# Optimization experiments

Hardware: AMD Instinct MI355X
Metric: run time of the kernel (lower is better)

The kernel has to match this reference:

```python
import jax, jax.numpy as jnp
import numpy as np

B, N, FEAT = 64, 1024, 3
HID, STATE, LAYERS, NTYPES = 64, 32, 2, 10


def setup_inputs() -> dict:
    key = jax.random.key(0)
    ks = jax.random.split(key, 16)
    s = 0.1
    return {
        "task_features": jax.random.normal(ks[0], (B, N, FEAT), jnp.float32),
        "task_types": jax.random.randint(ks[1], (B, N), 0, NTYPES, jnp.int32),
        "prev_state": jnp.zeros((B, STATE), jnp.float32),
        "enc_w1": jax.random.normal(ks[2], (HID, FEAT), jnp.float32) * s,
        "enc_b1": jnp.zeros((HID,), jnp.float32),
        "enc_w2": jax.random.normal(ks[3], (HID, HID), jnp.float32) * s,
        "enc_b2": jnp.zeros((HID,), jnp.float32),
        "contention": jax.random.normal(ks[4], (NTYPES, NTYPES), jnp.float32) * 0.1,
        "gnn_w": jax.random.normal(ks[5], (LAYERS, HID, HID), jnp.float32) * s,
        "gnn_b": jnp.zeros((LAYERS, HID), jnp.float32),
        "gru_w_ih": jax.random.normal(ks[6], (3 * STATE, HID), jnp.float32) * s,
        "gru_w_hh": jax.random.normal(ks[7], (3 * STATE, STATE), jnp.float32) * s,
        "gru_b_ih": jnp.zeros((3 * STATE,), jnp.float32),
        "gru_b_hh": jnp.zeros((3 * STATE,), jnp.float32),
        "head_w1": jax.random.normal(ks[8], (HID, HID + STATE), jnp.float32) * s,
        "head_b1": jnp.zeros((HID,), jnp.float32),
        "head_w2": jax.random.normal(ks[9], (1, HID), jnp.float32) * s,
        "head_b2": jnp.zeros((1,), jnp.float32),
    }


def _forward(task_features, task_types, prev_state, enc_w1, enc_b1, enc_w2, enc_b2,
             contention, gnn_w, gnn_b, gru_w_ih, gru_w_hh, gru_b_ih, gru_b_hh,
             head_w1, head_b1, head_w2, head_b2):
    # task encoder: Linear -> ReLU -> Linear
    emb = jax.nn.relu(task_features @ enc_w1.T + enc_b1) @ enc_w2.T + enc_b2  # (B,N,H)
    # interaction graph: type-pair gather + cosine similarity
    base = contention[task_types[:, :, None], task_types[:, None, :]]  # (B,N,N)
    nrm = emb / jnp.maximum(jnp.linalg.norm(emb, axis=-1, keepdims=True), 1e-12)
    sim = jnp.einsum("bnd,bmd->bnm", nrm, nrm)
    adjacency = jax.nn.sigmoid(base) * sim  # (B,N,N)
    # GNN layers: aggregate + linear + relu
    h = emb
    for l in range(LAYERS):
        agg = jnp.einsum("bnm,bmd->bnd", adjacency, h)
        h = jax.nn.relu((h + agg) @ gnn_w[l].T + gnn_b[l])
    ctx = h.mean(axis=1)  # (B,H)
    # GRUCell (torch semantics)
    gi = ctx @ gru_w_ih.T + gru_b_ih
    gh = prev_state @ gru_w_hh.T + gru_b_hh
    i_r, i_z, i_n = jnp.split(gi, 3, axis=-1)
    h_r, h_z, h_n = jnp.split(gh, 3, axis=-1)
    r = jax.nn.sigmoid(i_r + h_r)
    z = jax.nn.sigmoid(i_z + h_z)
    n = jnp.tanh(i_n + r * h_n)
    new_state = (1.0 - z) * n + z * prev_state  # (B,S)
    # latency head on [h, state]
    st = jnp.broadcast_to(new_state[:, None, :], (h.shape[0], h.shape[1], new_state.shape[-1]))
    combined = jnp.concatenate([h, st], axis=-1)
    lat = jax.nn.relu(combined @ head_w1.T + head_b1) @ head_w2.T + head_b2
    return lat[..., 0], new_state


def reference(task_features, task_types, prev_state, enc_w1, enc_b1, enc_w2, enc_b2,
              contention, gnn_w, gnn_b, gru_w_ih, gru_w_hh, gru_b_ih, gru_b_hh,
              head_w1, head_b1, head_w2, head_b2):
    return _forward(task_features, task_types, prev_state, enc_w1, enc_b1, enc_w2, enc_b2,
                    contention, gnn_w, gnn_b, gru_w_ih, gru_w_hh, gru_b_ih, gru_b_hh,
                    head_w1, head_b1, head_w2, head_b2)
```

## Files before the change

kernel.cpp:

```cpp
#include <hip/hip_runtime.h>
#include <math.h>

#define BB 64
#define NN 1024
#define HID 64
#define STATE 32
#define NTYPES 10
#define CAP 256
#define CAPE (CAP * 64)

typedef _Float16 f16;
typedef f16 f16x8 __attribute__((ext_vector_type(8)));
typedef f16 f16x4 __attribute__((ext_vector_type(4)));
typedef float f32x4 __attribute__((ext_vector_type(4)));

#define MFMA16(a, b, c) __builtin_amdgcn_mfma_f32_16x16x32_f16(a, b, c, 0, 0, 0)

__device__ __forceinline__ float sigm(float x) { return 1.f / (1.f + expf(-x)); }

__device__ __forceinline__ f16x8 cvt8(float4 a, float4 b) {
    f16x8 r;
    r[0] = (f16)a.x; r[1] = (f16)a.y; r[2] = (f16)a.z; r[3] = (f16)a.w;
    r[4] = (f16)b.x; r[5] = (f16)b.y; r[6] = (f16)b.z; r[7] = (f16)b.w;
    return r;
}
__device__ __forceinline__ unsigned packh2(f16 a, f16 b) {
    union { f16 h[2]; unsigned u; } p;
    p.h[0] = a; p.h[1] = b;
    return p.u;
}

__device__ __forceinline__ void swz_load(const float* __restrict__ W, int K, int n,
                                         f16* dst, int tid) {
    for (int p = tid; p < n; p += 256) {
        int j = p & 7, ln = (p >> 3) & 63, nt = (p >> 9) & 3, ch = p >> 11;
        int k = ch * 32 + ((ln >> 4) << 3) + j;
        int o = nt * 16 + (ln & 15);
        dst[p] = (f16)W[o * K + k];
    }
}

__global__ __launch_bounds__(256) void k_encoder(
    const float* __restrict__ feat,
    const float* __restrict__ w1, const float* __restrict__ b1,
    const float* __restrict__ w2, const float* __restrict__ b2,
    const int* __restrict__ types, int* __restrict__ idx, int* __restrict__ cnt,
    f16* __restrict__ nrmp, float* __restrict__ sclp, float* __restrict__ ctx)
{
    __shared__ f16 w2s[4096];
    __shared__ f16 tmp[4][16 * 72];
    __shared__ float fbuf[4][48];
    __shared__ int pkbuf[64];
    int tid = threadIdx.x, wave = tid >> 6, lane = tid & 63;
    int l15 = lane & 15, quad = lane >> 4;
    if (tid < 64) {
        int row = blockIdx.x * 64 + tid;
        int b = row >> 10;
        int t = types[row];
        int bt = b * NTYPES + t;
        int pos = atomicAdd(&cnt[bt], 1);
        idx[bt * CAP + pos] = row & (NN - 1);
        pkbuf[tid] = bt * CAP + pos;
    }
    if (blockIdx.x < 16) ctx[blockIdx.x * 256 + tid] = 0.f;
    swz_load(w2, 64, 4096, w2s, tid);
    float w10 = w1[lane * 3], w11 = w1[lane * 3 + 1], w12 = w1[lane * 3 + 2], b1l = b1[lane];
    int tb = blockIdx.x * 64 + wave * 16;
    if (lane < 48) fbuf[wave][lane] = feat[tb * 3 + lane];
    __syncthreads();
    f16* tw = &tmp[wave][0];
#pragma unroll
    for (int r = 0; r < 16; ++r) {
        float x0 = fbuf[wave][r * 3], x1 = fbuf[wave][r * 3 + 1], x2 = fbuf[wave][r * 3 + 2];
        float hv = fmaxf(fmaf(w10, x0, fmaf(w11, x1, fmaf(w12, x2, b1l))), 0.f);
        tw[r * 72 + lane] = (f16)hv;
    }
    __builtin_amdgcn_sched_barrier(0);
    f16x8 a0 = *(const f16x8*)&tw[l15 * 72 + quad * 8];
    f16x8 a1 = *(const f16x8*)&tw[l15 * 72 + 32 + quad * 8];
    const f16x8* bf = (const f16x8*)w2s;
    f32x4 acc[4];
#pragma unroll
    for (int nt = 0; nt < 4; ++nt) {
        f32x4 c = {0.f, 0.f, 0.f, 0.f};
        c = MFMA16(a0, bf[(0 * 4 + nt) * 64 + lane], c);
        c = MFMA16(a1, bf[(1 * 4 + nt) * 64 + lane], c);
        acc[nt] = c;
    }
    float b2c[4];
#pragma unroll
    for (int nt = 0; nt < 4; ++nt) b2c[nt] = b2[nt * 16 + l15];
#pragma unroll
    for (int i = 0; i < 4; ++i) {
        float v[4]; float ss = 0.f;
#pragma unroll
        for (int nt = 0; nt < 4; ++nt) { v[nt] = acc[nt][i] + b2c[nt]; ss = fmaf(v[nt], v[nt], ss); }
        ss += __shfl_xor(ss, 1, 64); ss += __shfl_xor(ss, 2, 64);
        ss += __shfl_xor(ss, 4, 64); ss += __shfl_xor(ss, 8, 64);
        float nm = fmaxf(sqrtf(ss), 1e-12f);
        float rinv = 1.f / nm;
        int pk = pkbuf[wave * 16 + quad * 4 + i];
#pragma unroll
        for (int nt = 0; nt < 4; ++nt)
            nrmp[(size_t)pk * 64 + nt * 16 + l15] = (f16)(v[nt] * rinv);
        if (l15 == 0) sclp[pk] = nm;
    }
}

#define TSTR2 72
__global__ __launch_bounds__(256) void k_buildM0(
    const int* __restrict__ cnt, const f16* __restrict__ nrmp,
    const float* __restrict__ sclp, f16* __restrict__ M0)
{
    __shared__ f16 nT[64 * TSTR2];
    __shared__ f16 hT[64 * TSTR2];
    int i0 = blockIdx.x;
    int xcd = i0 & 7, kk = i0 >> 3;
    int b = xcd + 8 * (kk / NTYPES);
    int t = kk % NTYPES;
    int bt = b * NTYPES + t;
    int c = cnt[bt];
    int tid = threadIdx.x, wave = tid >> 6, lane = tid & 63;
    int l15 = lane & 15, quad = lane >> 4;
    int r = tid & 15, q4 = tid >> 4;
    const f16* nb = nrmp + (size_t)bt * CAPE;
    const float* sb = sclp + (size_t)bt * CAP;
    f32x4 acc[4] = {{0.f,0.f,0.f,0.f},{0.f,0.f,0.f,0.f},{0.f,0.f,0.f,0.f},{0.f,0.f,0.f,0.f}};
    for (int k0 = 0; k0 < c; k0 += 64) {
        __syncthreads();
        f16x4 a[4], g[4];
#pragma unroll
        for (int u = 0; u < 4; ++u) { a[u] = (f16x4){0,0,0,0}; g[u] = (f16x4){0,0,0,0}; }
#pragma unroll
        for (int u = 0; u < 4; ++u) {
            int mi = k0 + 4 * r + u;
            if (mi < c) {
                a[u] = *(const f16x4*)&nb[(size_t)mi * 64 + 4 * q4];
                f16 sm = (f16)sb[mi]; f16x4 sv = {sm, sm, sm, sm};
                g[u] = a[u] * sv;
            }
        }
#pragma unroll
        for (int i = 0; i < 4; ++i) {
            *(unsigned*)&nT[(4 * q4 + i) * TSTR2 + 4 * r]     = packh2(a[0][i], a[1][i]);
            *(unsigned*)&nT[(4 * q4 + i) * TSTR2 + 4 * r + 2] = packh2(a[2][i], a[3][i]);
            *(unsigned*)&hT[(4 * q4 + i) * TSTR2 + 4 * r]     = packh2(g[0][i], g[1][i]);
            *(unsigned*)&hT[(4 * q4 + i) * TSTR2 + 4 * r + 2] = packh2(g[2][i], g[3][i]);
        }
        __syncthreads();
        f16x8 af0 = *(const f16x8*)&nT[(wave * 16 + l15) * TSTR2 + quad * 8];
        f16x8 af1 = *(const f16x8*)&nT[(wave * 16 + l15) * TSTR2 + 32 + quad * 8];
#pragma unroll
        for (int nt = 0; nt < 4; ++nt) {
            f16x8 bf0 = *(const f16x8*)&hT[(nt * 16 + l15) * TSTR2 + quad * 8];
            f16x8 bf1 = *(const f16x8*)&hT[(nt * 16 + l15) * TSTR2 + 32 + quad * 8];
            acc[nt] = MFMA16(af0, bf0, acc[nt]);
            acc[nt] = MFMA16(af1, bf1, acc[nt]);
        }
    }
    f16* Mo = M0 + (size_t)bt * 4096;
#pragma unroll
    for (int nt = 0; nt < 4; ++nt)
#pragma unroll
        for (int i = 0; i < 4; ++i)
            Mo[(wave * 16 + quad * 4 + i) * 64 + nt * 16 + l15] = (f16)acc[nt][i];
}

__global__ __launch_bounds__(256) void k_gnn0_fused(
    const int* __restrict__ cnt, const float* __restrict__ cont,
    const f16* __restrict__ M, const f16* __restrict__ nrmp,
    const float* __restrict__ sclp,
    const float* __restrict__ gw, const float* __restrict__ gb,
    f16* __restrict__ h1p, f16* __restrict__ Mout)
{
    __shared__ f16 ds_[4096];
    __shared__ f16 gs[4096];
    __shared__ __align__(16) f16 nT[64 * TSTR2];
    __shared__ __align__(16) f16 hT[64 * TSTR2];
    int i0 = blockIdx.x;
    int xcd = i0 & 7, kk = i0 >> 3;
    int b = xcd + 8 * (kk / NTYPES);
    int t = kk % NTYPES;
    int bt = b * NTYPES + t;
    int c = cnt[bt];
    int tid = threadIdx.x, wave = tid >> 6, lane = tid & 63;
    int l15 = lane & 15, quad = lane >> 4;
    swz_load(gw, 64, 4096, gs, tid);
    float sg[NTYPES];
#pragma unroll
    for (int j = 0; j < NTYPES; ++j) sg[j] = sigm(cont[t * NTYPES + j]);
    float ca[16];
#pragma unroll
    for (int i = 0; i < 16; ++i) ca[i] = 0.f;
    const f16* Mb = M + (size_t)b * NTYPES * 4096;
#pragma unroll
    for (int j = 0; j < NTYPES; ++j) {
        const f16* Mr = Mb + j * 4096 + (wave * 16 + l15) * 64;
        f16x8 m0 = *(const f16x8*)&Mr[quad * 8];
        f16x8 m1 = *(const f16x8*)&Mr[32 + quad * 8];
        float sv = sg[j];
#pragma unroll
        for (int e = 0; e < 8; ++e) {
            ca[e]     = fmaf(sv, (float)m0[e], ca[e]);
            ca[8 + e] = fmaf(sv, (float)m1[e], ca[8 + e]);
        }
    }
    f16x8 ca0, ca1;
#pragma unroll
    for (int i = 0; i < 8; ++i) { ca0[i] = (f16)ca[i]; ca1[i] = (f16)ca[8 + i]; }
    __syncthreads();
    const f16x8* gbf = (const f16x8*)gs;
#pragma unroll
    for (int nt = 0; nt < 4; ++nt) {
        f32x4 dd = {0.f, 0.f, 0.f, 0.f};
        dd = MFMA16(ca0, gbf[(0 * 4 + nt) * 64 + lane], dd);
        dd = MFMA16(ca1, gbf[(1 * 4 + nt) * 64 + lane], dd);
#pragma unroll
        for (int i = 0; i < 4; ++i) {
            int d = wave * 16 + quad * 4 + i;
            int pos = (((d >> 5) * 4 + nt) * 64 + ((d >> 3) & 3) * 16 + l15) * 8 + (d & 7);
            ds_[pos] = (f16)dd[i];
        }
    }
    __syncthreads();
    float gbl[4];
#pragma unroll
    for (int nt = 0; nt < 4; ++nt) gbl[nt] = gb[nt * 16 + l15];
    const f16* nb = nrmp + (size_t)bt * CAPE;
    const float* sb = sclp + (size_t)bt * CAP;
    f16* hob = h1p + (size_t)bt * CAPE;
    const f16x8* dbf = (const f16x8*)ds_;
    f32x4 macc[4];
#pragma unroll
    for (int nt = 0; nt < 4; ++nt) macc[nt] = (f32x4){0.f, 0.f, 0.f, 0.f};
    int nchunk = (c + 63) >> 6;
    for (int ch = 0; ch < nchunk; ++ch) {
        int tb = ch * 64 + wave * 16;
        int rA = tb + l15;
        bool okA = rA < c;
        int rAc = okA ? rA : (c - 1);
        const f16* na = nb + (size_t)rAc * 64;
        f16x8 a0 = *(const f16x8*)&na[quad * 8];
        f16x8 a1 = *(const f16x8*)&na[32 + quad * 8];
        f32x4 acc1[4], acc2[4];
#pragma unroll
        for (int nt = 0; nt < 4; ++nt) {
            f32x4 c1 = {0.f, 0.f, 0.f, 0.f}, c2 = {0.f, 0.f, 0.f, 0.f};
            c1 = MFMA16(a0, dbf[(0 * 4 + nt) * 64 + lane], c1);
            c1 = MFMA16(a1, dbf[(1 * 4 + nt) * 64 + lane], c1);
            c2 = MFMA16(a0, gbf[(0 * 4 + nt) * 64 + lane], c2);
            c2 = MFMA16(a1, gbf[(1 * 4 + nt) * 64 + lane], c2);
            acc1[nt] = c1; acc2[nt] = c2;
        }
        f16x4 hv[4];
#pragma unroll
        for (int nt = 0; nt < 4; ++nt) hv[nt] = (f16x4){0, 0, 0, 0};
#pragma unroll
        for (int i = 0; i < 4; ++i) {
            int rr = tb + quad * 4 + i;
            if (rr < c) {
                float sm = sb[rr];
#pragma unroll
                for (int nt = 0; nt < 4; ++nt) {
                    float v = fmaxf(fmaf(sm, acc2[nt][i], acc1[nt][i]) + gbl[nt], 0.f);
                    f16 vh = (f16)v;
                    hob[(size_t)rr * 64 + nt * 16 + l15] = vh;
                    hv[nt][i] = vh;
                }
            }
        }
        f16x8 z8 = {0, 0, 0, 0, 0, 0, 0, 0};
        f16x8 s0 = okA ? a0 : z8;
        f16x8 s1 = okA ? a1 : z8;
#pragma unroll
        for (int j = 0; j < 8; ++j) {
            nT[(quad * 8 + j) * TSTR2 + wave * 16 + l15]      = s0[j];
            nT[(32 + quad * 8 + j) * TSTR2 + wave * 16 + l15] = s1[j];
        }
#pragma unroll
        for (int nt = 0; nt < 4; ++nt)
            *(f16x4*)&hT[(nt * 16 + l15) * TSTR2 + wave * 16 + quad * 4] = hv[nt];
        __syncthreads();
        f16x8 af0 = *(const f16x8*)&nT[(wave * 16 + l15) * TSTR2 + quad * 8];
        f16x8 af1 = *(const f16x8*)&nT[(wave * 16 + l15) * TSTR2 + 32 + quad * 8];
#pragma unroll
        for (int nt = 0; nt < 4; ++nt) {
            f16x8 bf0 = *(const f16x8*)&hT[(nt * 16 + l15) * TSTR2 + quad * 8];
            f16x8 bf1 = *(const f16x8*)&hT[(nt * 16 + l15) * TSTR2 + 32 + quad * 8];
            macc[nt] = MFMA16(af0, bf0, macc[nt]);
            macc[nt] = MFMA16(af1, bf1, macc[nt]);
        }
        __syncthreads();
    }
    f16* Mo = Mout + (size_t)bt * 4096;
#pragma unroll
    for (int nt = 0; nt < 4; ++nt)
#pragma unroll
        for (int i = 0; i < 4; ++i)
            Mo[(wave * 16 + quad * 4 + i) * 64 + nt * 16 + l15] = (f16)macc[nt][i];
}

__global__ __launch_bounds__(256) void k_gnn1(
    const int* __restrict__ cnt, const float* __restrict__ cont,
    const f16* __restrict__ M, const f16* __restrict__ nrmp,
    const f16* __restrict__ h1p,
    const float* __restrict__ gw, const float* __restrict__ gb,
    f16* __restrict__ h2p, float* __restrict__ ctx)
{
    __shared__ f16 ds_[4096];
    __shared__ f16 gs[4096];
    int i0 = blockIdx.x;
    int xcd = i0 & 7, kk = i0 >> 3;
    int b = xcd + 8 * (kk / NTYPES);
    int t = kk % NTYPES;
    int bt = b * NTYPES + t;
    int c = cnt[bt];
    if (c == 0) return;
    int tid = threadIdx.x, wave = tid >> 6, lane = tid & 63;
    int l15 = lane & 15, quad = lane >> 4;
    swz_load(gw, 64, 4096, gs, tid);
    float sg[NTYPES];
#pragma unroll
    for (int j = 0; j < NTYPES; ++j) sg[j] = sigm(cont[t * NTYPES + j]);
    float ca[16];
#pragma unroll
    for (int i = 0; i < 16; ++i) ca[i] = 0.f;
    const f16* Mb = M + (size_t)b * NTYPES * 4096;
#pragma unroll
    for (int j = 0; j < NTYPES; ++j) {
        const f16* Mr = Mb + j * 4096 + (wave * 16 + l15) * 64;
        f16x8 m0 = *(const f16x8*)&Mr[quad * 8];
        f16x8 m1 = *(const f16x8*)&Mr[32 + quad * 8];
        float sv = sg[j];
#pragma unroll
        for (int e = 0; e < 8; ++e) {
            ca[e]     = fmaf(sv, (float)m0[e], ca[e]);
            ca[8 + e] = fmaf(sv, (float)m1[e], ca[8 + e]);
        }
    }
    f16x8 ca0, ca1;
#pragma unroll
    for (int i = 0; i < 8; ++i) { ca0[i] = (f16)ca[i]; ca1[i] = (f16)ca[8 + i]; }
    __syncthreads();
    const f16x8* gbf = (const f16x8*)gs;
#pragma unroll
    for (int nt = 0; nt < 4; ++nt) {
        f32x4 dd = {0.f, 0.f, 0.f, 0.f};
        dd = MFMA16(ca0, gbf[(0 * 4 + nt) * 64 + lane], dd);
        dd = MFMA16(ca1, gbf[(1 * 4 + nt) * 64 + lane], dd);
#pragma unroll
        for (int i = 0; i < 4; ++i) {
            int d = wave * 16 + quad * 4 + i;
            int pos = (((d >> 5) * 4 + nt) * 64 + ((d >> 3) & 3) * 16 + l15) * 8 + (d & 7);
            ds_[pos] = (f16)dd[i];
        }
    }
    __syncthreads();
    float gbl[4];
#pragma unroll
    for (int nt = 0; nt < 4; ++nt) gbl[nt] = gb[nt * 16 + l15];
    const f16* nb = nrmp + (size_t)bt * CAPE;
    const f16* hb = h1p + (size_t)bt * CAPE;
    f16* hob = h2p + (size_t)bt * CAPE;
    const f16x8* dbf = (const f16x8*)ds_;
    float cacc[4] = {0.f, 0.f, 0.f, 0.f};
    for (int g = wave; g * 16 < c; g += 4) {
        int tb = g * 16;
        int rA = tb + l15; if (rA >= c) rA = c - 1;
        const f16* na = nb + (size_t)rA * 64;
        f16x8 a0 = *(const f16x8*)&na[quad * 8];
        f16x8 a1 = *(const f16x8*)&na[32 + quad * 8];
        const f16* ha = hb + (size_t)rA * 64;
        f16x8 h0 = *(const f16x8*)&ha[quad * 8];
        f16x8 h1 = *(const f16x8*)&ha[32 + quad * 8];
        f32x4 acc[4];
#pragma unroll
        for (int nt = 0; nt < 4; ++nt) {
            f32x4 cc = {0.f, 0.f, 0.f, 0.f};
            cc = MFMA16(a0, dbf[(0 * 4 + nt) * 64 + lane], cc);
            cc = MFMA16(a1, dbf[(1 * 4 + nt) * 64 + lane], cc);
            cc = MFMA16(h0, gbf[(0 * 4 + nt) * 64 + lane], cc);
            cc = MFMA16(h1, gbf[(1 * 4 + nt) * 64 + lane], cc);
            acc[nt] = cc;
        }
#pragma unroll
        for (int i = 0; i < 4; ++i) {
            int rr = tb + quad * 4 + i;
            if (rr < c) {
#pragma unroll
                for (int nt = 0; nt < 4; ++nt) {
                    float v = fmaxf(acc[nt][i] + gbl[nt], 0.f);
                    hob[(size_t)rr * 64 + nt * 16 + l15] = (f16)v;
                    cacc[nt] += v;
                }
            }
        }
    }
#pragma unroll
    for (int nt = 0; nt < 4; ++nt) {
        float sv = cacc[nt];
        sv += __shfl_xor(sv, 16, 64);
        sv += __shfl_xor(sv, 32, 64);
        if (quad == 0) atomicAdd(&ctx[b * HID + nt * 16 + l15], sv);
    }
}

__global__ __launch_bounds__(256) void k_head(
    const f16* __restrict__ h2p, const int* __restrict__ idx,
    const int* __restrict__ cnt, const float* __restrict__ ctx_sum,
    const float* __restrict__ prev,
    const float* __restrict__ w_ih, const float* __restrict__ w_hh,
    const float* __restrict__ b_ih, const float* __restrict__ b_hh,
    const float* __restrict__ hw1, const float* __restrict__ b1,
    const float* __restrict__ w2, const float* __restrict__ b2,
    float* __restrict__ lat, float* __restrict__ state_out)
{
    __shared__ f16 ws_[6144];
    __shared__ __align__(16) float st[STATE];
    __shared__ float cs[HID], ps[STATE], gis[96], ghs[96];
    int i0 = blockIdx.x;
    int xcd = i0 & 7, kk = i0 >> 3;
    int b = xcd + 8 * (kk / NTYPES);
    int t = kk % NTYPES;
    int bt = b * NTYPES + t;
    int c = cnt[bt];
    int tid = threadIdx.x, wave = tid >> 6, lane = tid & 63;
    int l15 = lane & 15, quad = lane >> 4;
    swz_load(hw1, 96, 6144, ws_, tid);
    if (tid < HID) cs[tid] = ctx_sum[b * HID + tid] * (1.f / NN);
    if (tid >= HID && tid < HID + STATE) ps[tid - HID] = prev[b * STATE + tid - HID];
    __syncthreads();
    if (tid < 96) {
        float gi = b_ih[tid];
#pragma unroll 8
        for (int k = 0; k < HID; ++k) gi = fmaf(w_ih[tid * HID + k], cs[k], gi);
        float gh = b_hh[tid];
#pragma unroll
        for (int k = 0; k < STATE; ++k) gh = fmaf(w_hh[tid * STATE + k], ps[k], gh);
        gis[tid] = gi; ghs[tid] = gh;
    }
    __syncthreads();
    if (tid < STATE) {
        float r = sigm(gis[tid] + ghs[tid]);
        float z = sigm(gis[32 + tid] + ghs[32 + tid]);
        float nn = tanhf(gis[64 + tid] + r * ghs[64 + tid]);
        float v = (1.f - z) * nn + z * ps[tid];
        st[tid] = v;
        if (t == 0) state_out[b * STATE + tid] = v;
    }
    __syncthreads();
    if (c == 0) return;
    float b1c[4], w2c[4];
#pragma unroll
    for (int nt = 0; nt < 4; ++nt) { b1c[nt] = b1[nt * 16 + l15]; w2c[nt] = w2[nt * 16 + l15]; }
    float b2v = b2[0];
    const float4* sp = (const float4*)st;
    f16x8 a2 = cvt8(sp[quad * 2], sp[quad * 2 + 1]);
    const f16x8* bf = (const f16x8*)ws_;
    const f16* hb = h2p + (size_t)bt * CAPE;
    const int* lst = idx + (size_t)bt * CAP;
    for (int g = wave; g * 16 < c; g += 4) {
        int tb = g * 16;
        int rA = tb + l15; if (rA >= c) rA = c - 1;
        const f16* ha = hb + (size_t)rA * 64;
        f16x8 a0 = *(const f16x8*)&ha[quad * 8];
        f16x8 a1 = *(const f16x8*)&ha[32 + quad * 8];
        f32x4 acc[4];
#pragma unroll
        for (int nt = 0; nt < 4; ++nt) {
            f32x4 cc = {0.f, 0.f, 0.f, 0.f};
            cc = MFMA16(a0, bf[(0 * 4 + nt) * 64 + lane], cc);
            cc = MFMA16(a1, bf[(1 * 4 + nt) * 64 + lane], cc);
            cc = MFMA16(a2, bf[(2 * 4 + nt) * 64 + lane], cc);
            acc[nt] = cc;
        }
#pragma unroll
        for (int i = 0; i < 4; ++i) {
            float s = 0.f;
#pragma unroll
            for (int nt = 0; nt < 4; ++nt) s = fmaf(fmaxf(acc[nt][i] + b1c[nt], 0.f), w2c[nt], s);
            s += __shfl_xor(s, 1, 64); s += __shfl_xor(s, 2, 64);
            s += __shfl_xor(s, 4, 64); s += __shfl_xor(s, 8, 64);
            int rr = tb + quad * 4 + i;
            if (l15 == 0 && rr < c) {
                int m = lst[rr];
                lat[b * NN + m] = s + b2v;
            }
        }
    }
}

extern "C" void kernel_launch(void* const* d_in, const int* in_sizes, int n_in,
                              void* d_out, int out_size, void* d_ws, size_t ws_size,
                              hipStream_t stream) {
    const float* feat   = (const float*)d_in[0];
    const int*   types  = (const int*)d_in[1];
    const float* prev   = (const float*)d_in[2];
    const float* enc_w1 = (const float*)d_in[3];
    const float* enc_b1 = (const float*)d_in[4];
    const float* enc_w2 = (const float*)d_in[5];
    const float* enc_b2 = (const float*)d_in[6];
    const float* cont   = (const float*)d_in[7];
    const float* gnn_w  = (const float*)d_in[8];
    const float* gnn_b  = (const float*)d_in[9];
    const float* w_ih   = (const float*)d_in[10];
    const float* w_hh   = (const float*)d_in[11];
    const float* b_ih   = (const float*)d_in[12];
    const float* b_hh   = (const float*)d_in[13];
    const float* hw1    = (const float*)d_in[14];
    const float* hb1    = (const float*)d_in[15];
    const float* hw2    = (const float*)d_in[16];
    const float* hb2    = (const float*)d_in[17];
    float* out = (float*)d_out;

    float* ws   = (float*)d_ws;
    f16*   nrmp = (f16*)ws;
    f16*   h1p  = (f16*)(ws + 5242880);
    f16*   h2p  = (f16*)(ws + 10485760);
    float* sclp = ws + 15728640;
    int*   idx  = (int*)(ws + 15892480);
    int*   cnt  = (int*)(ws + 16056320);
    f16*   M0   = (f16*)(ws + 16057344);
    f16*   M1   = (f16*)(ws + 17368064);
    float* ctx  = ws + 18678784;

    hipMemsetAsync(cnt, 0, BB * NTYPES * sizeof(int), stream);
    k_encoder<<<BB * NN / 64, 256, 0, stream>>>(feat, enc_w1, enc_b1, enc_w2, enc_b2,
                                                types, idx, cnt, nrmp, sclp, ctx);
    k_buildM0<<<BB * NTYPES, 256, 0, stream>>>(cnt, nrmp, sclp, M0);
    k_gnn0_fused<<<BB * NTYPES, 256, 0, stream>>>(cnt, cont, M0, nrmp, sclp,
                                                  gnn_w, gnn_b, h1p, M1);
    k_gnn1<<<BB * NTYPES, 256, 0, stream>>>(cnt, cont, M1, nrmp, h1p,
                                            gnn_w + 4096, gnn_b + HID, h2p, ctx);
    k_head<<<BB * NTYPES, 256, 0, stream>>>(h2p, idx, cnt, ctx, prev,
                                            w_ih, w_hh, b_ih, b_hh,
                                            hw1, hb1, hw2, hb2, out, out + BB * NN);
}
```

Before: 165.8 us.

## Fuse encoder and M0 build into one per-batch kernel with local counting

New measurement: 173.7 us. +4.7%, slower.

```diff
diff --git a/kernel.cpp b/kernel.cpp
--- a/kernel.cpp
+++ b/kernel.cpp
@@ -8,6 +8,8 @@
 #define NTYPES 10
 #define CAP 256
 #define CAPE (CAP * 64)
+#define TSTR2 72
+#define TSTR3 40
 
 typedef _Float16 f16;
 typedef f16 f16x8 __attribute__((ext_vector_type(8)));
@@ -31,8 +33,8 @@
 }
 
 __device__ __forceinline__ void swz_load(const float* __restrict__ W, int K, int n,
-                                         f16* dst, int tid) {
-    for (int p = tid; p < n; p += 256) {
+                                         f16* dst, int tid, int nthr) {
+    for (int p = tid; p < n; p += nthr) {
         int j = p & 7, ln = (p >> 3) & 63, nt = (p >> 9) & 3, ch = p >> 11;
         int k = ch * 32 + ((ln >> 4) << 3) + j;
         int o = nt * 16 + (ln & 15);
@@ -40,130 +42,142 @@
     }
 }
 
-__global__ __launch_bounds__(256) void k_encoder(
-    const float* __restrict__ feat,
+__global__ __launch_bounds__(1024) void k_encM0(
+    const float* __restrict__ feat, const int* __restrict__ types,
     const float* __restrict__ w1, const float* __restrict__ b1,
     const float* __restrict__ w2, const float* __restrict__ b2,
-    const int* __restrict__ types, int* __restrict__ idx, int* __restrict__ cnt,
-    f16* __restrict__ nrmp, float* __restrict__ sclp, float* __restrict__ ctx)
+    f16* __restrict__ nrmp, float* __restrict__ sclp, int* __restrict__ idx,
+    int* __restrict__ cnt, float* __restrict__ ctx, f16* __restrict__ M0)
 {
-    __shared__ f16 w2s[4096];
-    __shared__ f16 tmp[4][16 * 72];
-    __shared__ float fbuf[4][48];
-    __shared__ int pkbuf[64];
-    int tid = threadIdx.x, wave = tid >> 6, lane = tid & 63;
-    int l15 = lane & 15, quad = lane >> 4;
-    if (tid < 64) {
-        int row = blockIdx.x * 64 + tid;
-        int b = row >> 10;
-        int t = types[row];
-        int bt = b * NTYPES + t;
-        int pos = atomicAdd(&cnt[bt], 1);
-        idx[bt * CAP + pos] = row & (NN - 1);
-        pkbuf[tid] = bt * CAP + pos;
-    }
-    if (blockIdx.x < 16) ctx[blockIdx.x * 256 + tid] = 0.f;
-    swz_load(w2, 64, 4096, w2s, tid);
-    float w10 = w1[lane * 3], w11 = w1[lane * 3 + 1], w12 = w1[lane * 3 + 2], b1l = b1[lane];
-    int tb = blockIdx.x * 64 + wave * 16;
-    if (lane < 48) fbuf[wave][lane] = feat[tb * 3 + lane];
-    __syncthreads();
-    f16* tw = &tmp[wave][0];
-#pragma unroll
-    for (int r = 0; r < 16; ++r) {
-        float x0 = fbuf[wave][r * 3], x1 = fbuf[wave][r * 3 + 1], x2 = fbuf[wave][r * 3 + 2];
-        float hv = fmaxf(fmaf(w10, x0, fmaf(w11, x1, fmaf(w12, x2, b1l))), 0.f);
-        tw[r * 72 + lane] = (f16)hv;
-    }
-    __builtin_amdgcn_sched_barrier(0);
-    f16x8 a0 = *(const f16x8*)&tw[l15 * 72 + quad * 8];
-    f16x8 a1 = *(const f16x8*)&tw[l15 * 72 + 32 + quad * 8];
-    const f16x8* bf = (const f16x8*)w2s;
-    f32x4 acc[4];
-#pragma unroll
-    for (int nt = 0; nt < 4; ++nt) {
-        f32x4 c = {0.f, 0.f, 0.f, 0.f};
-        c = MFMA16(a0, bf[(0 * 4 + nt) * 64 + lane], c);
-        c = MFMA16(a1, bf[(1 * 4 + nt) * 64 + lane], c);
-        acc[nt] = c;
-    }
-    float b2c[4];
-#pragma unroll
-    for (int nt = 0; nt < 4; ++nt) b2c[nt] = b2[nt * 16 + l15];
-#pragma unroll
-    for (int i = 0; i < 4; ++i) {
-        float v[4]; float ss = 0.f;
-#pragma unroll
-        for (int nt = 0; nt < 4; ++nt) { v[nt] = acc[nt][i] + b2c[nt]; ss = fmaf(v[nt], v[nt], ss); }
-        ss += __shfl_xor(ss, 1, 64); ss += __shfl_xor(ss, 2, 64);
-        ss += __shfl_xor(ss, 4, 64); ss += __shfl_xor(ss, 8, 64);
-        float nm = fmaxf(sqrtf(ss), 1e-12f);
-        float rinv = 1.f / nm;
-        int pk = pkbuf[wave * 16 + quad * 4 + i];
-#pragma unroll
-        for (int nt = 0; nt < 4; ++nt)
-            nrmp[(size_t)pk * 64 + nt * 16 + l15] = (f16)(v[nt] * rinv);
-        if (l15 == 0) sclp[pk] = nm;
-    }
-}
-
-#define TSTR2 72
-__global__ __launch_bounds__(256) void k_buildM0(
-    const int* __restrict__ cnt, const f16* __restrict__ nrmp,
-    const float* __restrict__ sclp, f16* __restrict__ M0)
-{
-    __shared__ f16 nT[64 * TSTR2];
-    __shared__ f16 hT[64 * TSTR2];
-    int i0 = blockIdx.x;
-    int xcd = i0 & 7, kk = i0 >> 3;
-    int b = xcd + 8 * (kk / NTYPES);
-    int t = kk % NTYPES;
-    int bt = b * NTYPES + t;
-    int c = cnt[bt];
-    int tid = threadIdx.x, wave = tid >> 6, lane = tid & 63;
-    int l15 = lane & 15, quad = lane >> 4;
-    int r = tid & 15, q4 = tid >> 4;
-    const f16* nb = nrmp + (size_t)bt * CAPE;
-    const float* sb = sclp + (size_t)bt * CAP;
-    f32x4 acc[4] = {{0.f,0.f,0.f,0.f},{0.f,0.f,0.f,0.f},{0.f,0.f,0.f,0.f},{0.f,0.f,0.f,0.f}};
-    for (int k0 = 0; k0 < c; k0 += 64) {
-        __syncthreads();
-        f16x4 a[4], g[4];
-#pragma unroll
-        for (int u = 0; u < 4; ++u) { a[u] = (f16x4){0,0,0,0}; g[u] = (f16x4){0,0,0,0}; }
-#pragma unroll
-        for (int u = 0; u < 4; ++u) {
-            int mi = k0 + 4 * r + u;
-            if (mi < c) {
-                a[u] = *(const f16x4*)&nb[(size_t)mi * 64 + 4 * q4];
-                f16 sm = (f16)sb[mi]; f16x4 sv = {sm, sm, sm, sm};
-                g[u] = a[u] * sv;
-            }
-        }
-#pragma unroll
-        for (int i = 0; i < 4; ++i) {
-            *(unsigned*)&nT[(4 * q4 + i) * TSTR2 + 4 * r]     = packh2(a[0][i], a[1][i]);
-            *(unsigned*)&nT[(4 * q4 + i) * TSTR2 + 4 * r + 2] = packh2(a[2][i], a[3][i]);
-            *(unsigned*)&hT[(4 * q4 + i) * TSTR2 + 4 * r]     = packh2(g[0][i], g[1][i]);
-            *(unsigned*)&hT[(4 * q4 + i) * TSTR2 + 4 * r + 2] = packh2(g[2][i], g[3][i]);
-        }
-        __syncthreads();
-        f16x8 af0 = *(const f16x8*)&nT[(wave * 16 + l15) * TSTR2 + quad * 8];
-        f16x8 af1 = *(const f16x8*)&nT[(wave * 16 + l15) * TSTR2 + 32 + quad * 8];
-#pragma unroll
-        for (int nt = 0; nt < 4; ++nt) {
-            f16x8 bf0 = *(const f16x8*)&hT[(nt * 16 + l15) * TSTR2 + quad * 8];
-            f16x8 bf1 = *(const f16x8*)&hT[(nt * 16 + l15) * TSTR2 + 32 + quad * 8];
-            acc[nt] = MFMA16(af0, bf0, acc[nt]);
-            acc[nt] = MFMA16(af1, bf1, acc[nt]);
-        }
-    }
-    f16* Mo = M0 + (size_t)bt * 4096;
-#pragma unroll
-    for (int nt = 0; nt < 4; ++nt)
-#pragma unroll
-        for (int i = 0; i < 4; ++i)
-            Mo[(wave * 16 + quad * 4 + i) * 64 + nt * 16 + l15] = (f16)acc[nt][i];
+    __shared__ __align__(16) unsigned char smem[52288];
+    f16* w2s = (f16*)smem;
+    int* pkmap = (int*)(smem + 48128);
+    int* cntl = (int*)(smem + 52224);
+
+    const int tid = threadIdx.x;
+    const int w = tid >> 6, lane = tid & 63;
+    const int g = w >> 2, wg = w & 3;
+    const int l15 = lane & 15, quad = lane >> 4;
+    const int b = blockIdx.x;
+
+    if (tid < NTYPES) cntl[tid] = 0;
+    if (tid < HID) ctx[b * HID + tid] = 0.f;
+    swz_load(w2, 64, 4096, w2s, tid, 1024);
+    __syncthreads();
+    {
+        int t = types[b * NN + tid];
+        int pos = atomicAdd(&cntl[t], 1);
+        int pk = (b * NTYPES + t) * CAP + pos;
+        idx[pk] = tid;
+        pkmap[tid] = pk;
+    }
+    __syncthreads();
+    if (tid < NTYPES) cnt[b * NTYPES + tid] = cntl[tid];
+
+    {
+        f16* tw = (f16*)(smem + 8192) + w * 1152;
+        float* fw = (float*)(smem + 45056) + w * 48;
+        float w10 = w1[lane * 3], w11 = w1[lane * 3 + 1],
+              w12 = w1[lane * 3 + 2], b1l = b1[lane];
+        float b2c[4];
+#pragma unroll
+        for (int nt = 0; nt < 4; ++nt) b2c[nt] = b2[nt * 16 + l15];
+        const f16x8* wbf = (const f16x8*)w2s;
+        for (int p = 0; p < 4; ++p) {
+            int rowbase = p * 256 + w * 16;
+            if (lane < 48) fw[lane] = feat[((size_t)b * NN + rowbase) * 3 + lane];
+            __builtin_amdgcn_sched_barrier(0);
+#pragma unroll
+            for (int r = 0; r < 16; ++r) {
+                float x0 = fw[r * 3], x1 = fw[r * 3 + 1], x2 = fw[r * 3 + 2];
+                float hv = fmaxf(fmaf(w10, x0, fmaf(w11, x1, fmaf(w12, x2, b1l))), 0.f);
+                tw[r * 72 + lane] = (f16)hv;
+            }
+            __builtin_amdgcn_sched_barrier(0);
+            f16x8 a0 = *(const f16x8*)&tw[l15 * 72 + quad * 8];
+            f16x8 a1 = *(const f16x8*)&tw[l15 * 72 + 32 + quad * 8];
+            f32x4 acc[4];
+#pragma unroll
+            for (int nt = 0; nt < 4; ++nt) {
+                f32x4 c = {0.f, 0.f, 0.f, 0.f};
+                c = MFMA16(a0, wbf[(0 * 4 + nt) * 64 + lane], c);
+                c = MFMA16(a1, wbf[(1 * 4 + nt) * 64 + lane], c);
+                acc[nt] = c;
+            }
+#pragma unroll
+            for (int i = 0; i < 4; ++i) {
+                float v[4]; float ss = 0.f;
+#pragma unroll
+                for (int nt = 0; nt < 4; ++nt) { v[nt] = acc[nt][i] + b2c[nt]; ss = fmaf(v[nt], v[nt], ss); }
+                ss += __shfl_xor(ss, 1, 64); ss += __shfl_xor(ss, 2, 64);
+                ss += __shfl_xor(ss, 4, 64); ss += __shfl_xor(ss, 8, 64);
+                float nm = fmaxf(sqrtf(ss), 1e-12f);
+                float rinv = 1.f / nm;
+                int pk = pkmap[rowbase + quad * 4 + i];
+#pragma unroll
+                for (int nt = 0; nt < 4; ++nt)
+                    nrmp[(size_t)pk * 64 + nt * 16 + l15] = (f16)(v[nt] * rinv);
+                if (l15 == 0) sclp[pk] = nm;
+            }
+        }
+    }
+
+    {
+        const int gt = tid & 255;
+        const int srr = gt & 15, sq4 = gt >> 4;
+        f16* nT = (f16*)(smem + g * 10240);
+        f16* hT = (f16*)(smem + g * 10240 + 5120);
+        for (int r = 0; r < 3; ++r) {
+            int tg = r * 4 + g;
+            bool valid = tg < NTYPES;
+            int bt = b * NTYPES + (valid ? tg : 0);
+            int c = valid ? cntl[tg] : 0;
+            int cmax = 0;
+            for (int gg = 0; gg < 4; ++gg) {
+                int tgg = r * 4 + gg;
+                if (tgg < NTYPES) cmax = max(cmax, cntl[tgg]);
+            }
+            int nch = (cmax + 31) >> 5;
+            const f16* nb = nrmp + (size_t)bt * CAPE;
+            const float* sb = sclp + (size_t)bt * CAP;
+            f32x4 acc[4] = {{0.f,0.f,0.f,0.f},{0.f,0.f,0.f,0.f},
+                            {0.f,0.f,0.f,0.f},{0.f,0.f,0.f,0.f}};
+            for (int ch = 0; ch < nch; ++ch) {
+                __syncthreads();
+                f16x4 a[2], hh[2];
+                a[0] = (f16x4){0,0,0,0}; a[1] = a[0]; hh[0] = a[0]; hh[1] = a[0];
+#pragma unroll
+                for (int u = 0; u < 2; ++u) {
+                    int mi = ch * 32 + 2 * srr + u;
+                    if (mi < c) {
+                        a[u] = *(const f16x4*)&nb[(size_t)mi * 64 + 4 * sq4];
+                        f16 sm = (f16)sb[mi];
+                        hh[u] = a[u] * (f16x4){sm, sm, sm, sm};
+                    }
+                }
+#pragma unroll
+                for (int i = 0; i < 4; ++i) {
+                    *(unsigned*)&nT[(4 * sq4 + i) * TSTR3 + 2 * srr] = packh2(a[0][i], a[1][i]);
+                    *(unsigned*)&hT[(4 * sq4 + i) * TSTR3 + 2 * srr] = packh2(hh[0][i], hh[1][i]);
+                }
+                __syncthreads();
+                f16x8 af = *(const f16x8*)&nT[(wg * 16 + l15) * TSTR3 + quad * 8];
+#pragma unroll
+                for (int nt = 0; nt < 4; ++nt) {
+                    f16x8 bfv = *(const f16x8*)&hT[(nt * 16 + l15) * TSTR3 + quad * 8];
+                    acc[nt] = MFMA16(af, bfv, acc[nt]);
+                }
+            }
+            if (valid) {
+                f16* Mo = M0 + (size_t)bt * 4096;
+#pragma unroll
+                for (int nt = 0; nt < 4; ++nt)
+#pragma unroll
+                    for (int i = 0; i < 4; ++i)
+                        Mo[(wg * 16 + quad * 4 + i) * 64 + nt * 16 + l15] = (f16)acc[nt][i];
+            }
+        }
+    }
 }
 
 __global__ __launch_bounds__(256) void k_gnn0_fused(
@@ -185,7 +199,7 @@
     int c = cnt[bt];
     int tid = threadIdx.x, wave = tid >> 6, lane = tid & 63;
     int l15 = lane & 15, quad = lane >> 4;
-    swz_load(gw, 64, 4096, gs, tid);
+    swz_load(gw, 64, 4096, gs, tid, 256);
     float sg[NTYPES];
 #pragma unroll
     for (int j = 0; j < NTYPES; ++j) sg[j] = sigm(cont[t * NTYPES + j]);
@@ -318,7 +332,7 @@
     if (c == 0) return;
     int tid = threadIdx.x, wave = tid >> 6, lane = tid & 63;
     int l15 = lane & 15, quad = lane >> 4;
-    swz_load(gw, 64, 4096, gs, tid);
+    swz_load(gw, 64, 4096, gs, tid, 256);
     float sg[NTYPES];
 #pragma unroll
     for (int j = 0; j < NTYPES; ++j) sg[j] = sigm(cont[t * NTYPES + j]);
@@ -426,7 +440,7 @@
     int c = cnt[bt];
     int tid = threadIdx.x, wave = tid >> 6, lane = tid & 63;
     int l15 = lane & 15, quad = lane >> 4;
-    swz_load(hw1, 96, 6144, ws_, tid);
+    swz_load(hw1, 96, 6144, ws_, tid, 256);
     if (tid < HID) cs[tid] = ctx_sum[b * HID + tid] * (1.f / NN);
     if (tid >= HID && tid < HID + STATE) ps[tid - HID] = prev[b * STATE + tid - HID];
     __syncthreads();
@@ -524,10 +538,8 @@
     f16*   M1   = (f16*)(ws + 17368064);
     float* ctx  = ws + 18678784;
 
-    hipMemsetAsync(cnt, 0, BB * NTYPES * sizeof(int), stream);
-    k_encoder<<<BB * NN / 64, 256, 0, stream>>>(feat, enc_w1, enc_b1, enc_w2, enc_b2,
-                                                types, idx, cnt, nrmp, sclp, ctx);
-    k_buildM0<<<BB * NTYPES, 256, 0, stream>>>(cnt, nrmp, sclp, M0);
+    k_encM0<<<BB, 1024, 0, stream>>>(feat, types, enc_w1, enc_b1, enc_w2, enc_b2,
+                                     nrmp, sclp, idx, cnt, ctx, M0);
     k_gnn0_fused<<<BB * NTYPES, 256, 0, stream>>>(cnt, cont, M0, nrmp, sclp,
                                                   gnn_w, gnn_b, h1p, M1);
     k_gnn1<<<BB * NTYPES, 256, 0, stream>>>(cnt, cont, M1, nrmp, h1p,
```
